# Kernel optimization log

Measured on AMD Instinct MI355X. Metric: run time of the kernel, lower is better.

Reference implementation:

```python
import jax, jax.numpy as jnp
import numpy as np

N_HEADS = 8
N_POINTS = 4


def _grid_sample_bilinear(img, x, y):
    """PyTorch-style grid_sample, mode='bilinear', align_corners=True, zeros padding.
    img: [G, D, Hk, Wk]; x, y: [G, P] pixel coords. Returns [G, D, P]."""
    G, D, Hk, Wk = img.shape
    x0 = jnp.floor(x); y0 = jnp.floor(y)
    x1 = x0 + 1.0; y1 = y0 + 1.0
    wx1 = x - x0; wx0 = 1.0 - wx1
    wy1 = y - y0; wy0 = 1.0 - wy1
    imgf = img.reshape(G, D, Hk * Wk)

    def corner(xi, yi, w):
        valid = (xi >= 0) & (xi <= Wk - 1) & (yi >= 0) & (yi <= Hk - 1)
        ix = jnp.clip(xi, 0, Wk - 1).astype(jnp.int32)
        iy = jnp.clip(yi, 0, Hk - 1).astype(jnp.int32)
        idx = iy * Wk + ix  # [G, P]
        g = jax.vmap(lambda im, i: jnp.take(im, i, axis=1))(imgf, idx)  # [G, D, P]
        return g * (w * valid.astype(w.dtype))[:, None, :]

    return (corner(x0, y0, wx0 * wy0) + corner(x1, y0, wx1 * wy0)
            + corner(x0, y1, wx0 * wy1) + corner(x1, y1, wx1 * wy1))


def setup_inputs() -> dict:
    key = jax.random.key(0)
    ks = jax.random.split(key, 6)
    B, C, H, W = 8, 256, 64, 64
    return {
        "query": jax.random.normal(ks[0], (B, C, H, W), jnp.float32),
        "key": jax.random.normal(ks[1], (B, C, H, W), jnp.float32),
        "w_off": jax.random.normal(ks[2], (N_HEADS * N_POINTS * 3, C), jnp.float32) * 0.02,
        "b_off": jax.random.normal(ks[3], (N_HEADS * N_POINTS * 3,), jnp.float32) * 0.02,
        "w_proj": jax.random.normal(ks[4], (C, C), jnp.float32) * 0.02,
        "b_proj": jax.random.normal(ks[5], (C,), jnp.float32) * 0.02,
    }


def reference(query, key, w_off, b_off, w_proj, b_proj):
    B, C, H, W = query.shape
    Hk, Wk = key.shape[2], key.shape[3]
    d_head = C // N_HEADS

    # [B, N, C]
    q = query.reshape(B, C, H * W).transpose(0, 2, 1)
    ow = q @ w_off.T + b_off                      # [B, N, heads*points*3]
    ow = ow.reshape(B, H, W, N_HEADS, N_POINTS, 3)
    offsets = ow[..., :2]                          # [B,H,W,h,p,2]
    wts = jax.nn.softmax(ow[..., 2], axis=-1)      # [B,H,W,h,p]

    gy, gx = jnp.meshgrid(jnp.linspace(-1.0, 1.0, H, dtype=query.dtype),
                          jnp.linspace(-1.0, 1.0, W, dtype=query.dtype), indexing='ij')
    grid = jnp.stack([gx, gy], axis=-1).reshape(1, H, W, 1, 1, 2)
    locs = grid + offsets * 0.1                    # [B,H,W,h,p,2] normalized coords
    locs = locs.transpose(0, 3, 4, 1, 2, 5)        # [B,h,p,H,W,2]

    G = B * N_HEADS
    locs = locs.reshape(G, N_POINTS * H * W, 2)
    xg = (locs[..., 0] + 1.0) * 0.5 * (Wk - 1)     # align_corners=True mapping
    yg = (locs[..., 1] + 1.0) * 0.5 * (Hk - 1)

    key_r = key.reshape(G, d_head, Hk, Wk)
    sampled = _grid_sample_bilinear(key_r, xg, yg)            # [G, d_head, p*H*W]
    sampled = sampled.reshape(B, N_HEADS, d_head, N_POINTS, H, W)

    w = wts.transpose(0, 3, 4, 1, 2)               # [B,h,p,H,W]
    out_feat = jnp.einsum('bhdpxy,bhpxy->bhdxy', sampled, w)  # [B,h,d,H,W]
    out_feat = out_feat.reshape(B, C, H * W).transpose(0, 2, 1)  # [B,N,C]
    return out_feat @ w_proj.T + b_proj
```

## Files before the change

### kernel.cpp

```cpp
#include <hip/hip_runtime.h>
#include <cstdint>

#define B_   8
#define C_   256
#define H_   64
#define W_   64
#define HW_  4096
#define NH_  8
#define NP_  4
#define DH_  32

typedef unsigned int u32;
typedef unsigned short u16;
typedef __attribute__((ext_vector_type(8))) short bf16x8;
typedef __attribute__((ext_vector_type(4))) float f32x4;
typedef __attribute__((ext_vector_type(4))) u32 u32x4;
typedef __attribute__((address_space(3))) u32 as3_u32;
typedef __attribute__((address_space(1))) u32 as1_u32;

__device__ __forceinline__ u16 f2bf(float f) {
  u32 u = __builtin_bit_cast(u32, f);
  return (u16)((u + 0x7FFFu + ((u >> 16) & 1u)) >> 16);
}
__device__ __forceinline__ float bflo(u32 v) { return __builtin_bit_cast(float, v << 16); }
__device__ __forceinline__ float bfhi(u32 v) { return __builtin_bit_cast(float, v & 0xFFFF0000u); }

__global__ __launch_bounds__(256) void k_trans_conv(const float* __restrict__ key,
                                                    const float* __restrict__ w_proj,
                                                    u32* __restrict__ key_t2,
                                                    uint2* __restrict__ wproj_bf) {
  __shared__ float tile[32 * 65];
  const int bid = blockIdx.x;
  const int t = threadIdx.x;

  if (bid < 4096) {
    const int g = bid >> 6;
    const int hw0 = (bid & 63) << 6;
    const float* kg = key + (size_t)g * DH_ * HW_ + hw0;
    #pragma unroll
    for (int k = 0; k < 8; ++k) {
      int idx = t + k * 256;
      int d = idx >> 6, j = idx & 63;
      tile[d * 65 + j] = kg[d * HW_ + j];
    }
    __syncthreads();
    u32* kt = key_t2 + ((size_t)g * HW_ + hw0) * 16;
    #pragma unroll
    for (int k = 0; k < 4; ++k) {
      int idx = t + k * 256;
      int j = idx >> 4, dp = idx & 15;
      u32 v = (u32)f2bf(tile[(2 * dp) * 65 + j]) | ((u32)f2bf(tile[(2 * dp + 1) * 65 + j]) << 16);
      kt[j * 16 + dp] = v;
    }
  } else {
    int i = (bid - 4096) * 256 + t;
    float4 v = ((const float4*)w_proj)[i];
    uint2 o;
    o.x = (u32)f2bf(v.x) | ((u32)f2bf(v.y) << 16);
    o.y = (u32)f2bf(v.z) | ((u32)f2bf(v.w) << 16);
    wproj_bf[i] = o;
  }
}

__global__ __launch_bounds__(256) void k_offsets_mfma(const float* __restrict__ query,
                                                      const float* __restrict__ w_off,
                                                      const float* __restrict__ b_off,
                                                      float4* __restrict__ wts4,
                                                      u32* __restrict__ idx4) {
  __shared__ char smem[57344];
  const int t = threadIdx.x, l = t & 63, w = t >> 6;
  const int lr = l & 15, lq = l >> 4;
  const int r0 = blockIdx.x * 128;
  const int b  = r0 >> 12;
  const int hw0 = r0 & 4095;

  {
    const float4* w4 = (const float4*)w_off;
    #pragma unroll
    for (int j = 0; j < 12; ++j) {
      int m = t + j * 256;
      int col = m >> 5, ch = m & 31;
      float4 lo = w4[m * 2];
      float4 hi = w4[m * 2 + 1];
      u32x4 v;
      v.x = (u32)f2bf(lo.x) | ((u32)f2bf(lo.y) << 16);
      v.y = (u32)f2bf(lo.z) | ((u32)f2bf(lo.w) << 16);
      v.z = (u32)f2bf(hi.x) | ((u32)f2bf(hi.y) << 16);
      v.w = (u32)f2bf(hi.z) | ((u32)f2bf(hi.w) << 16);
      int slot = (col << 5) | (ch ^ (col & 7));
      *(u32x4*)(smem + slot * 16) = v;
    }
  }

  f32x4 acc[2][6];
  #pragma unroll
  for (int m = 0; m < 2; ++m)
    #pragma unroll
    for (int n = 0; n < 6; ++n)
      acc[m][n] = (f32x4){0.f, 0.f, 0.f, 0.f};

  for (int step = 0; step < 8; ++step) {
    const int k0 = step * 32;
    #pragma unroll
    for (int it = 0; it < 8; ++it) {
      int idx = t + it * 256;
      int i = idx & 127;
      int p = idx >> 7;
      const float* src = query + ((size_t)(b * 256 + k0 + 2 * p)) * 4096 + hw0 + i;
      u32 v = (u32)f2bf(src[0]) | ((u32)f2bf(src[4096]) << 16);
      *(u32*)(smem + 49152 + ((p >> 2) * 128 + i) * 16 + (p & 3) * 4) = v;
    }
    __syncthreads();

    const int chb = step * 4 + lq;
    bf16x8 bfr[6], af[2];
    #pragma unroll
    for (int n = 0; n < 6; ++n) {
      int col = n * 16 + lr;
      bfr[n] = *(const bf16x8*)(smem + ((col << 5) | (chb ^ (col & 7))) * 16);
    }
    #pragma unroll
    for (int m = 0; m < 2; ++m)
      af[m] = *(const bf16x8*)(smem + 49152 + (lq * 128 + w * 32 + m * 16 + lr) * 16);

    #pragma unroll
    for (int m = 0; m < 2; ++m)
      #pragma unroll
      for (int n = 0; n < 6; ++n)
        acc[m][n] = __builtin_amdgcn_mfma_f32_16x16x32_bf16(af[m], bfr[n], acc[m][n], 0, 0, 0);
    __syncthreads();
  }

  float* epi = (float*)smem;
  #pragma unroll
  for (int n = 0; n < 6; ++n) {
    int o = n * 16 + lr;
    float bo = b_off[o];
    #pragma unroll
    for (int m = 0; m < 2; ++m) {
      int row = w * 32 + m * 16 + lq * 4;
      #pragma unroll
      for (int r = 0; r < 4; ++r)
        epi[(row + r) * 98 + o] = acc[m][n][r] + bo;
    }
  }
  __syncthreads();

  #pragma unroll
  for (int k = 0; k < 4; ++k) {
    int task = t + k * 256;
    int row = task & 127, head = task >> 7;
    const float* o = epi + row * 98 + head * 12;
    float ox[NP_], oy[NP_], lg[NP_];
    #pragma unroll
    for (int p = 0; p < NP_; ++p) {
      ox[p] = o[p * 3 + 0];
      oy[p] = o[p * 3 + 1];
      lg[p] = o[p * 3 + 2];
    }
    float mx = fmaxf(fmaxf(lg[0], lg[1]), fmaxf(lg[2], lg[3]));
    float e[NP_];
    float s = 0.f;
    #pragma unroll
    for (int p = 0; p < NP_; ++p) { e[p] = expf(lg[p] - mx); s += e[p]; }
    float inv = 1.f / s;

    int hw = (r0 + row) & 4095;
    float wq = (float)(hw & 63);
    float hq = (float)(hw >> 6);
    size_t base = ((size_t)(b * NH_ + head) * HW_ + hw) * NP_;
    #pragma unroll
    for (int p = 0; p < NP_; ++p) {
      float wt = e[p] * inv;
      float x = wq + ox[p] * 3.15f;
      float y = hq + oy[p] * 3.15f;
      float x0f = floorf(x), y0f = floorf(y);
      int ix0 = (int)x0f, iy0 = (int)y0f;
      int ix1 = ix0 + 1, iy1 = iy0 + 1;
      float fx = x - x0f, fy = y - y0f;
      float gx0 = 1.f - fx, gy0 = 1.f - fy;

      bool vx0 = (ix0 >= 0) & (ix0 <= W_ - 1);
      bool vx1 = (ix1 >= 0) & (ix1 <= W_ - 1);
      bool vy0 = (iy0 >= 0) & (iy0 <= H_ - 1);
      bool vy1 = (iy1 >= 0) & (iy1 <= H_ - 1);
      int cx0 = min(max(ix0, 0), W_ - 1), cx1 = min(max(ix1, 0), W_ - 1);
      int cy0 = min(max(iy0, 0), H_ - 1), cy1 = min(max(iy1, 0), H_ - 1);

      float4 ww;
      ww.x = wt * gx0 * gy0 * ((vx0 & vy0) ? 1.f : 0.f);
      ww.y = wt * fx  * gy0 * ((vx1 & vy0) ? 1.f : 0.f);
      ww.z = wt * gx0 * fy  * ((vx0 & vy1) ? 1.f : 0.f);
      ww.w = wt * fx  * fy  * ((vx1 & vy1) ? 1.f : 0.f);
      wts4[base + p] = ww;
      idx4[base + p] = (u32)cx0 | ((u32)cx1 << 6) | ((u32)cy0 << 12) | ((u32)cy1 << 18);
    }
  }
}

__global__ __launch_bounds__(256) void k_sample(const float4* __restrict__ wts4,
                                                const u32* __restrict__ idx4,
                                                const u32* __restrict__ key_t2,
                                                u32* __restrict__ feat2) {
  const int t = threadIdx.x;
  const int hwid = blockIdx.x * 2 + (t >> 7);
  const int b = hwid >> 12;
  const int hw = hwid & 4095;
  const int c2 = t & 127;
  const int head = c2 >> 4, dp = c2 & 15;
  const int g = b * NH_ + head;
  const size_t pbase = (((size_t)g << 12) + hw) * NP_;
  const u32* kg = key_t2 + ((size_t)g << 16) + dp;

  float4 W[NP_];
  u32 I[NP_];
  #pragma unroll
  for (int p = 0; p < NP_; ++p) { W[p] = wts4[pbase + p]; I[p] = idx4[pbase + p]; }

  u32 v00[NP_], v01[NP_], v10[NP_], v11[NP_];
  #pragma unroll
  for (int p = 0; p < NP_; ++p) {
    u32 ip = I[p];
    int cx0 = ip & 63, cx1 = (ip >> 6) & 63, cy0 = (ip >> 12) & 63, cy1 = (ip >> 18) & 63;
    v00[p] = kg[((cy0 << 6) | cx0) * 16];
    v01[p] = kg[((cy0 << 6) | cx1) * 16];
    v10[p] = kg[((cy1 << 6) | cx0) * 16];
    v11[p] = kg[((cy1 << 6) | cx1) * 16];
  }

  float a0 = 0.f, a1 = 0.f;
  #pragma unroll
  for (int p = 0; p < NP_; ++p) {
    a0 = fmaf(W[p].x, bflo(v00[p]), a0);
    a0 = fmaf(W[p].y, bflo(v01[p]), a0);
    a0 = fmaf(W[p].z, bflo(v10[p]), a0);
    a0 = fmaf(W[p].w, bflo(v11[p]), a0);
    a1 = fmaf(W[p].x, bfhi(v00[p]), a1);
    a1 = fmaf(W[p].y, bfhi(v01[p]), a1);
    a1 = fmaf(W[p].z, bfhi(v10[p]), a1);
    a1 = fmaf(W[p].w, bfhi(v11[p]), a1);
  }
  feat2[((size_t)b * HW_ + hw) * 128 + c2] = (u32)f2bf(a0) | ((u32)f2bf(a1) << 16);
}

__global__ __launch_bounds__(256) void k_proj_mfma(const u16* __restrict__ A,
                                                   const u16* __restrict__ Bw,
                                                   const float* __restrict__ bias,
                                                   float* __restrict__ out) {
  __shared__ char smem[16384];
  const int t = threadIdx.x, w = t >> 6, l = t & 63;
  const int wm = w >> 1, wn = w & 1;
  const int bid = blockIdx.x;
  const int nb = bid & 1, mb = bid >> 1;
  const int r0 = mb * 128, n0 = nb * 128;

  f32x4 acc[4][4];
  #pragma unroll
  for (int m = 0; m < 4; ++m)
    #pragma unroll
    for (int n = 0; n < 4; ++n)
      acc[m][n] = (f32x4){0.f, 0.f, 0.f, 0.f};

  for (int k0 = 0; k0 < 256; k0 += 32) {
    if (w < 2) {
      #pragma unroll
      for (int j = 0; j < 4; ++j) {
        int i = w * 4 + j;
        int kq = i >> 1, half = i & 1;
        const u16* g = A + ((size_t)(r0 + half * 64 + l)) * 256 + k0 + kq * 8;
        __builtin_amdgcn_global_load_lds((const as1_u32*)g, (as3_u32*)(smem + i * 1024), 16, 0, 0);
      }
    } else {
      #pragma unroll
      for (int j = 0; j < 4; ++j) {
        int i = (w - 2) * 4 + j;
        int kq = i >> 1, half = i & 1;
        const u16* g = Bw + ((size_t)(n0 + half * 64 + l)) * 256 + k0 + kq * 8;
        __builtin_amdgcn_global_load_lds((const as1_u32*)g, (as3_u32*)(smem + 8192 + i * 1024), 16, 0, 0);
      }
    }
    __syncthreads();

    const int kq = l >> 4, lr = l & 15;
    bf16x8 af[4], bfr[4];
    #pragma unroll
    for (int m = 0; m < 4; ++m)
      af[m] = *(const bf16x8*)(smem + (kq * 128 + wm * 64 + m * 16 + lr) * 16);
    #pragma unroll
    for (int n = 0; n < 4; ++n)
      bfr[n] = *(const bf16x8*)(smem + 8192 + (kq * 128 + wn * 64 + n * 16 + lr) * 16);
    #pragma unroll
    for (int m = 0; m < 4; ++m)
      #pragma unroll
      for (int n = 0; n < 4; ++n)
        acc[m][n] = __builtin_amdgcn_mfma_f32_16x16x32_bf16(af[m], bfr[n], acc[m][n], 0, 0, 0);
    __syncthreads();
  }

  const int lr = l & 15, lq = l >> 4;
  #pragma unroll
  for (int n = 0; n < 4; ++n) {
    int col = n0 + wn * 64 + n * 16 + lr;
    float bv = bias[col];
    #pragma unroll
    for (int m = 0; m < 4; ++m) {
      int row = r0 + wm * 64 + m * 16 + lq * 4;
      #pragma unroll
      for (int r = 0; r < 4; ++r)
        out[(size_t)(row + r) * 256 + col] = acc[m][n][r] + bv;
    }
  }
}

extern "C" void kernel_launch(void* const* d_in, const int* in_sizes, int n_in,
                              void* d_out, int out_size, void* d_ws, size_t ws_size,
                              hipStream_t stream) {
  const float* query  = (const float*)d_in[0];
  const float* key    = (const float*)d_in[1];
  const float* w_off  = (const float*)d_in[2];
  const float* b_off  = (const float*)d_in[3];
  const float* w_proj = (const float*)d_in[4];
  const float* b_proj = (const float*)d_in[5];
  float* out = (float*)d_out;

  char* ws = (char*)d_ws;
  float4* wts4     = (float4*)ws;
  u32*    key_t2   = (u32*)(ws + (size_t)16 * 1024 * 1024);
  u32*    idx4     = (u32*)(ws + (size_t)32 * 1024 * 1024);
  u32*    feat2    = (u32*)(ws + (size_t)36 * 1024 * 1024);
  uint2*  wproj_bf = (uint2*)(ws + (size_t)52 * 1024 * 1024);

  hipLaunchKernelGGL(k_trans_conv,  dim3(4160),  dim3(256), 0, stream,
                     key, w_proj, key_t2, wproj_bf);
  hipLaunchKernelGGL(k_offsets_mfma, dim3(256),  dim3(256), 0, stream,
                     query, w_off, b_off, wts4, idx4);
  hipLaunchKernelGGL(k_sample,      dim3(16384), dim3(256), 0, stream,
                     wts4, idx4, key_t2, feat2);
  hipLaunchKernelGGL(k_proj_mfma,   dim3(512),   dim3(256), 0, stream,
                     (const u16*)feat2, (const u16*)wproj_bf, b_proj, out);
}
```

Before: 71.82 us.

## Halve offset-GEMM row tile and preload full query K slab into LDS

The offset projection kernel now handles 64 rows per block instead of 128, doubling the grid to 512 blocks so more CUs are busy. It also loads the whole 256-channel query slab into shared memory once, instead of staging 32 channels per step with two barriers each. This removes per-step synchronisation and lets the MFMA loop run unrolled without stalls. In exchange, LDS use grows to 80KB per block, which limits occupancy, and the w_off conversion into LDS is repeated by twice as many blocks.

```diff
diff --git a/kernel.cpp b/kernel.cpp
--- a/kernel.cpp
+++ b/kernel.cpp
@@ -67,10 +67,10 @@
                                                       const float* __restrict__ b_off,
                                                       float4* __restrict__ wts4,
                                                       u32* __restrict__ idx4) {
-  __shared__ char smem[57344];
+  __shared__ char smem[81920];
   const int t = threadIdx.x, l = t & 63, w = t >> 6;
   const int lr = l & 15, lq = l >> 4;
-  const int r0 = blockIdx.x * 128;
+  const int r0 = blockIdx.x * 64;
   const int b  = r0 >> 12;
   const int hw0 = r0 & 4095;
 
@@ -92,64 +92,54 @@
     }
   }
 
-  f32x4 acc[2][6];
-  #pragma unroll
-  for (int m = 0; m < 2; ++m)
-    #pragma unroll
-    for (int n = 0; n < 6; ++n)
-      acc[m][n] = (f32x4){0.f, 0.f, 0.f, 0.f};
-
+  {
+    const float* qb = query + ((size_t)b * 256) * 4096 + hw0;
+    #pragma unroll
+    for (int it = 0; it < 32; ++it) {
+      int idx = t + it * 256;
+      int i = idx & 63;
+      int p = idx >> 6;
+      const float* src = qb + (size_t)(2 * p) * 4096 + i;
+      u32 v = (u32)f2bf(src[0]) | ((u32)f2bf(src[4096]) << 16);
+      int kc = p >> 2;
+      *(u32*)(smem + 49152 + (kc * 64 + i) * 16 + (p & 3) * 4) = v;
+    }
+  }
+  __syncthreads();
+
+  f32x4 acc[6];
+  #pragma unroll
+  for (int n = 0; n < 6; ++n) acc[n] = (f32x4){0.f, 0.f, 0.f, 0.f};
+
+  #pragma unroll
   for (int step = 0; step < 8; ++step) {
-    const int k0 = step * 32;
-    #pragma unroll
-    for (int it = 0; it < 8; ++it) {
-      int idx = t + it * 256;
-      int i = idx & 127;
-      int p = idx >> 7;
-      const float* src = query + ((size_t)(b * 256 + k0 + 2 * p)) * 4096 + hw0 + i;
-      u32 v = (u32)f2bf(src[0]) | ((u32)f2bf(src[4096]) << 16);
-      *(u32*)(smem + 49152 + ((p >> 2) * 128 + i) * 16 + (p & 3) * 4) = v;
-    }
-    __syncthreads();
-
-    const int chb = step * 4 + lq;
-    bf16x8 bfr[6], af[2];
+    const int kc = step * 4 + lq;
+    bf16x8 af = *(const bf16x8*)(smem + 49152 + (kc * 64 + w * 16 + lr) * 16);
     #pragma unroll
     for (int n = 0; n < 6; ++n) {
       int col = n * 16 + lr;
-      bfr[n] = *(const bf16x8*)(smem + ((col << 5) | (chb ^ (col & 7))) * 16);
-    }
-    #pragma unroll
-    for (int m = 0; m < 2; ++m)
-      af[m] = *(const bf16x8*)(smem + 49152 + (lq * 128 + w * 32 + m * 16 + lr) * 16);
-
-    #pragma unroll
-    for (int m = 0; m < 2; ++m)
-      #pragma unroll
-      for (int n = 0; n < 6; ++n)
-        acc[m][n] = __builtin_amdgcn_mfma_f32_16x16x32_bf16(af[m], bfr[n], acc[m][n], 0, 0, 0);
-    __syncthreads();
-  }
+      bf16x8 bfr = *(const bf16x8*)(smem + ((col << 5) | (kc ^ (col & 7))) * 16);
+      acc[n] = __builtin_amdgcn_mfma_f32_16x16x32_bf16(af, bfr, acc[n], 0, 0, 0);
+    }
+  }
+  __syncthreads();
 
   float* epi = (float*)smem;
   #pragma unroll
   for (int n = 0; n < 6; ++n) {
     int o = n * 16 + lr;
     float bo = b_off[o];
-    #pragma unroll
-    for (int m = 0; m < 2; ++m) {
-      int row = w * 32 + m * 16 + lq * 4;
-      #pragma unroll
-      for (int r = 0; r < 4; ++r)
-        epi[(row + r) * 98 + o] = acc[m][n][r] + bo;
-    }
+    int row = w * 16 + lq * 4;
+    #pragma unroll
+    for (int r = 0; r < 4; ++r)
+      epi[(row + r) * 98 + o] = acc[n][r] + bo;
   }
   __syncthreads();
 
   #pragma unroll
-  for (int k = 0; k < 4; ++k) {
+  for (int k = 0; k < 2; ++k) {
     int task = t + k * 256;
-    int row = task & 127, head = task >> 7;
+    int row = task & 63, head = task >> 6;
     const float* o = epi + row * 98 + head * 12;
     float ox[NP_], oy[NP_], lg[NP_];
     #pragma unroll
@@ -330,12 +320,12 @@
   u32*    feat2    = (u32*)(ws + (size_t)36 * 1024 * 1024);
   uint2*  wproj_bf = (uint2*)(ws + (size_t)52 * 1024 * 1024);
 
-  hipLaunchKernelGGL(k_trans_conv,  dim3(4160),  dim3(256), 0, stream,
+  hipLaunchKernelGGL(k_trans_conv,   dim3(4160),  dim3(256), 0, stream,
                      key, w_proj, key_t2, wproj_bf);
-  hipLaunchKernelGGL(k_offsets_mfma, dim3(256),  dim3(256), 0, stream,
+  hipLaunchKernelGGL(k_offsets_mfma, dim3(512),   dim3(256), 0, stream,
                      query, w_off, b_off, wts4, idx4);
-  hipLaunchKernelGGL(k_sample,      dim3(16384), dim3(256), 0, stream,
+  hipLaunchKernelGGL(k_sample,       dim3(16384), dim3(256), 0, stream,
                      wts4, idx4, key_t2, feat2);
-  hipLaunchKernelGGL(k_proj_mfma,   dim3(512),   dim3(256), 0, stream,
+  hipLaunchKernelGGL(k_proj_mfma,    dim3(512),   dim3(256), 0, stream,
                      (const u16*)feat2, (const u16*)wproj_bf, b_proj, out);
 }
```

After: 69.80 us. 2.8% less time.
